# Kernel optimization log

Hardware: AMD Instinct MI355X
Metric: run time of the kernel (lower is better)

Reference implementation:

```python
import jax, jax.numpy as jnp
import numpy as np

BETA = 0.25
N_E = 8192
E_DIM = 256


def setup_inputs() -> dict:
    key = jax.random.key(0)
    k1, k2 = jax.random.split(key)
    z = jax.random.normal(k1, (16, E_DIM, 32, 32), dtype=jnp.float32)
    # matches torch init: uniform_(-1/n_e, 1/n_e)
    codebook = jax.random.uniform(k2, (N_E, E_DIM), dtype=jnp.float32,
                                  minval=-1.0 / N_E, maxval=1.0 / N_E)
    return {"z": z, "codebook": codebook}


def reference(z, codebook):
    B, C, H, W = z.shape  # C == e_dim
    zp = jnp.transpose(z, (0, 2, 3, 1))          # [B, H, W, C]
    zf = zp.reshape(-1, C)                       # [N, C], N = B*H*W
    # squared L2 distances: ||z||^2 + ||e||^2 - 2 z.e
    d = (jnp.sum(zf * zf, axis=1, keepdims=True)
         + jnp.sum(codebook * codebook, axis=1)
         - 2.0 * jnp.einsum('nc,kc->nk', zf, codebook))  # [N, n_e]
    min_encoding_indices = jnp.argmin(d, axis=1)         # [N]
    z_q = codebook[min_encoding_indices].reshape(zp.shape)  # [B, H, W, C]
    sg = jax.lax.stop_gradient
    loss = jnp.mean((sg(z_q) - zp) ** 2) + BETA * jnp.mean((z_q - sg(zp)) ** 2)
    # straight-through estimator
    z_q_st = zp + sg(z_q - zp)
    z_q_out = jnp.transpose(z_q_st, (0, 3, 1, 2))  # back to NCHW
    return z_q_out, loss, min_encoding_indices
```

## Files before the change

### kernel.cpp

```cpp
#include <hip/hip_runtime.h>

typedef short s8v __attribute__((ext_vector_type(8)));
typedef float f4v __attribute__((ext_vector_type(4)));
typedef float f4 __attribute__((ext_vector_type(4)));
typedef unsigned short u16v4 __attribute__((ext_vector_type(4)));

#define N_PIX 16384
#define NE    8192
#define EDIM  256
#define ZQ_ELEMS 4194304
#define MARGIN 4.5e-4f
#define NGRP 512

__device__ __forceinline__ float bf2f(unsigned short u) {
    union { unsigned int i; float f; } c; c.i = ((unsigned int)u) << 16; return c.f;
}
__device__ __forceinline__ unsigned short f2bf(float f) {
    unsigned int u = __float_as_uint(f);
    u = (u + 0x7fffu + ((u >> 16) & 1u)) >> 16;
    return (unsigned short)u;
}
__device__ __forceinline__ unsigned short f2bf_down(float f) {
    unsigned int u = __float_as_uint(f);
    unsigned short b = (unsigned short)(u >> 16);
    if ((u & 0xFFFFu) && (u >> 31)) b += 1;
    return b;
}

__device__ __forceinline__ float np_pw128sq(const float* a) {
    float r[8];
    #pragma unroll
    for (int j = 0; j < 8; ++j) r[j] = __fmul_rn(a[j], a[j]);
    for (int i = 8; i < 128; i += 8)
        #pragma unroll
        for (int j = 0; j < 8; ++j) r[j] = __fadd_rn(r[j], __fmul_rn(a[i + j], a[i + j]));
    return __fadd_rn(__fadd_rn(__fadd_rn(r[0], r[1]), __fadd_rn(r[2], r[3])),
                     __fadd_rn(__fadd_rn(r[4], r[5]), __fadd_rn(r[6], r[7])));
}


__global__ __launch_bounds__(256) void vq_prep(const float* __restrict__ cb,
                                               unsigned short* __restrict__ cb16,
                                               float* __restrict__ esum32) {
    int t = threadIdx.x;
    int base = blockIdx.x * 32;
    const float* src = cb + (size_t)base * EDIM;
    unsigned short* dst = cb16 + (size_t)base * EDIM;
    #pragma unroll
    for (int i = 0; i < 8; ++i) {
        int e0 = (i * 256 + t) * 4;
        f4 v = *(const f4*)(src + e0);
        u16v4 o;
        o.x = f2bf(v[0]); o.y = f2bf(v[1]); o.z = f2bf(v[2]); o.w = f2bf(v[3]);
        *(u16v4*)(dst + e0) = o;
    }
    if (t < 32) {
        const float* a = cb + (size_t)(base + t) * EDIM;
        esum32[base + t] = __fadd_rn(np_pw128sq(a), np_pw128sq(a + 128));
    }
}

__global__ __launch_bounds__(256) void vq_zprep(const float* __restrict__ z,
                                                unsigned short* __restrict__ z16) {
    __shared__ unsigned short zl[64 * 66];
    int t = threadIdx.x;
    int p0 = (blockIdx.x >> 2) * 64;
    int c0 = (blockIdx.x & 3) * 64;
    int b = p0 >> 10, hw0 = p0 & 1023;
    const float* src = z + (((size_t)b * 256 + c0) << 10) + hw0;
    #pragma unroll
    for (int i = 0; i < 16; ++i) {
        int idx = i * 256 + t;
        int ch = idx >> 6, px = idx & 63;
        zl[px * 66 + ch] = f2bf(src[((size_t)ch << 10) + px]);
    }
    __syncthreads();
    #pragma unroll
    for (int i = 0; i < 16; ++i) {
        int idx = i * 256 + t;
        int px = idx >> 6, ch = idx & 63;
        z16[((size_t)(p0 + px)) * 256 + c0 + ch] = zl[px * 66 + ch];
    }
}

__global__ __launch_bounds__(512, 2) void vq_phase1g(const unsigned short* __restrict__ cb16,
                                                     const unsigned short* __restrict__ z16,
                                                     unsigned short* __restrict__ gmin) {
    __shared__ unsigned short L[2][32768];
    const int t = threadIdx.x;
    const int wave = t >> 6, lane = t & 63;
    const int q = lane >> 4, r = lane & 15;
    const int wr = wave >> 2, wc = wave & 3;
    const int cm0 = ((int)blockIdx.x >> 3) * 256;
    const int pg  = (int)blockIdx.x & 7;

    const int pc0 = t, pc1 = t + 512;
    const int row0 = pc0 >> 2, row1 = pc1 >> 2;
    const int lc0 = (pc0 & 3) ^ ((row0 >> 1) & 3);
    const int lc1 = (pc1 & 3) ^ ((row1 >> 1) & 3);
    const int go0 = row0 * 256 + lc0 * 8;
    const int go1 = row1 * 256 + lc1 * 8;
    const int ld0 = pc0 * 8;
    const int ld1 = pc1 * 8;

    const unsigned short* gA = cb16 + (size_t)cm0 * 256;
    const unsigned short* gB0 = z16 + (size_t)pg * 2048 * 256;

    f4v acc[8][4];
    const f4v zz = {0.f, 0.f, 0.f, 0.f};
    #pragma unroll
    for (int mi = 0; mi < 8; ++mi)
        #pragma unroll
        for (int ni = 0; ni < 4; ++ni) acc[mi][ni] = zz;

    const int cxo = (q ^ ((r >> 1) & 3)) * 8;
    const int aro = (wr * 128 + r) * 32 + cxo;
    const int bro = 16384 + (wc * 64 + r) * 32 + cxo;

#define GLL(g, l) __builtin_amdgcn_global_load_lds( \
        (const __attribute__((address_space(1))) unsigned int*)(g), \
        (__attribute__((address_space(3))) unsigned int*)(l), 16, 0, 0)
#define STAGEKT(buf_, gk_, gBp_) do { \
        unsigned short* Lb = &L[(buf_)][0]; \
        GLL(gA + go0 + (gk_),            Lb + ld0); \
        GLL(gA + go1 + (gk_),            Lb + ld1); \
        GLL(gA + go0 + 32 + (gk_),       Lb + 8192 + ld0); \
        GLL(gA + go1 + 32 + (gk_),       Lb + 8192 + ld1); \
        GLL((gBp_) + go0 + (gk_),        Lb + 16384 + ld0); \
        GLL((gBp_) + go1 + (gk_),        Lb + 16384 + ld1); \
        GLL((gBp_) + go0 + 32 + (gk_),   Lb + 16384 + 8192 + ld0); \
        GLL((gBp_) + go1 + 32 + (gk_),   Lb + 16384 + 8192 + ld1); } while (0)
#define ARD(Lp, mi, ks) (*(const s8v*)&(Lp)[(ks) * 8192 + (mi) * 512 + aro])
#define BRD(Lp, ni, ks) (*(const s8v*)&(Lp)[(ks) * 8192 + (ni) * 512 + bro])
#define MFMA16(Aset, Bset, mo) do { \
        __builtin_amdgcn_s_setprio(1); \
        _Pragma("unroll") \
        for (int mi = 0; mi < 4; ++mi) \
            _Pragma("unroll") \
            for (int ni = 0; ni < 4; ++ni) \
                acc[(mo) + mi][ni] = __builtin_amdgcn_mfma_f32_16x16x32_bf16( \
                    Aset[mi], Bset[ni], acc[(mo) + mi][ni], 0, 0, 0); \
        __builtin_amdgcn_s_setprio(0); } while (0)

    STAGEKT(0, 0, gB0);
    asm volatile("s_waitcnt vmcnt(0)" ::: "memory");
    __builtin_amdgcn_s_barrier();
    s8v A0[4], A1[4], B0[4], B1[4];
    #pragma unroll
    for (int ni = 0; ni < 4; ++ni) B0[ni] = BRD(&L[0][0], ni, 0);
    #pragma unroll
    for (int mi = 0; mi < 4; ++mi) A0[mi] = ARD(&L[0][0], mi, 0);

    for (int it = 0; it < 32; ++it) {
        const int buf = it & 1;
        const unsigned short* Lb = &L[buf][0];
        const unsigned short* Ln = &L[buf ^ 1][0];
        const int nit = it + 1;
        const bool st = nit < 32;

        __builtin_amdgcn_s_barrier();
        if (st) STAGEKT(buf ^ 1, (nit & 3) * 64, gB0 + (size_t)(nit >> 2) * 65536);

        #pragma unroll
        for (int mi = 0; mi < 4; ++mi) A1[mi] = ARD(Lb, 4 + mi, 0);
        __builtin_amdgcn_sched_barrier(0);
        MFMA16(A0, B0, 0);

        #pragma unroll
        for (int mi = 0; mi < 4; ++mi) A0[mi] = ARD(Lb, mi, 1);
        #pragma unroll
        for (int ni = 0; ni < 4; ++ni) B1[ni] = BRD(Lb, ni, 1);
        __builtin_amdgcn_sched_barrier(0);
        MFMA16(A1, B0, 4);

        #pragma unroll
        for (int mi = 0; mi < 4; ++mi) A1[mi] = ARD(Lb, 4 + mi, 1);
        __builtin_amdgcn_sched_barrier(0);
        MFMA16(A0, B1, 0);

        if (st) {
            asm volatile("s_waitcnt vmcnt(0)" ::: "memory");
            __builtin_amdgcn_s_barrier();
            #pragma unroll
            for (int ni = 0; ni < 4; ++ni) B0[ni] = BRD(Ln, ni, 0);
            #pragma unroll
            for (int mi = 0; mi < 4; ++mi) A0[mi] = ARD(Ln, mi, 0);
        }
        __builtin_amdgcn_sched_barrier(0);
        MFMA16(A1, B1, 4);

        if ((it & 3) == 3) {
            const int pn0 = pg * 2048 + (it >> 2) * 256;
            #pragma unroll
            for (int mi = 0; mi < 8; ++mi) {
                int g = cm0 / 16 + wr * 8 + mi;
                #pragma unroll
                for (int ni = 0; ni < 4; ++ni) {
                    f4v a = acc[mi][ni];
                    float mx = fmaxf(fmaxf(a[0], a[1]), fmaxf(a[2], a[3]));
                    mx = fmaxf(mx, __shfl_xor(mx, 16));
                    mx = fmaxf(mx, __shfl_xor(mx, 32));
                    if (q == 0) {
                        int pxc = (pn0 + wc * 64 + ni * 16) >> 4;
                        gmin[(size_t)pxc * 8192 + g * 16 + r] = f2bf_down(-2.0f * mx);
                    }
                    acc[mi][ni] = zz;
                }
            }
        }
    }
#undef MFMA16
#undef BRD
#undef ARD
#undef STAGEKT
#undef GLL
}

__global__ __launch_bounds__(512, 2) void vq_phase1(const float* __restrict__ z,
                                                    const unsigned short* __restrict__ cb16,
                                                    unsigned short* __restrict__ gmin) {
    const int t = threadIdx.x;
    const int wave = t >> 6, lane = t & 63;
    const int col = lane & 15, q = lane >> 4;
    const int mb = (blockIdx.x >> 1) * 64;
    const int chalf = blockIdx.x & 1;

    s8v Z[4][8];
    #pragma unroll
    for (int pt = 0; pt < 4; ++pt) {
        int n = mb + pt * 16 + col;
        const float* zb = z + ((size_t)(n >> 10) << 18) + (size_t)(n & 1023);
        #pragma unroll
        for (int c0 = 0; c0 < 8; ++c0) {
            s8v a;
            #pragma unroll
            for (int j = 0; j < 8; ++j) {
                int c = c0 * 32 + q * 8 + j;
                a[j] = (short)f2bf(zb[(size_t)c << 10]);
            }
            Z[pt][c0] = a;
        }
    }

    const int kbase = chalf * 4096 + wave * 512;
    for (int it = 0; it < 16; ++it) {
        int n0 = kbase + it * 32;
        const unsigned short* bb = cb16 + (size_t)(n0 + col) * EDIM + q * 8;
        f4v zz = {0.f, 0.f, 0.f, 0.f};
        f4v acc[4][2];
        #pragma unroll
        for (int pt = 0; pt < 4; ++pt) { acc[pt][0] = zz; acc[pt][1] = zz; }
        #pragma unroll
        for (int c0 = 0; c0 < 8; ++c0) {
            s8v C0 = *(const s8v*)(bb + c0 * 32);
            s8v C1 = *(const s8v*)(bb + 16 * EDIM + c0 * 32);
            #pragma unroll
            for (int pt = 0; pt < 4; ++pt) {
                acc[pt][0] = __builtin_amdgcn_mfma_f32_16x16x32_bf16(C0, Z[pt][c0], acc[pt][0], 0, 0, 0);
                acc[pt][1] = __builtin_amdgcn_mfma_f32_16x16x32_bf16(C1, Z[pt][c0], acc[pt][1], 0, 0, 0);
            }
        }
        int gbase = chalf * 256 + wave * 32 + it * 2;
        #pragma unroll
        for (int pt = 0; pt < 4; ++pt) {
            #pragma unroll
            for (int s = 0; s < 2; ++s) {
                f4v a = acc[pt][s];
                float mx = fmaxf(fmaxf(a[0], a[1]), fmaxf(a[2], a[3]));
                mx = fmaxf(mx, __shfl_xor(mx, 16));
                mx = fmaxf(mx, __shfl_xor(mx, 32));
                if (q == 0)
                    gmin[(size_t)((mb >> 4) + pt) * 8192 + (gbase + s) * 16 + col] =
                        f2bf_down(-2.0f * mx);
            }
        }
    }
}

__global__ __launch_bounds__(256) void vq_phase2(const float* __restrict__ z,
                                                 const float* __restrict__ cb,
                                                 const float* __restrict__ esum32,
                                                 const unsigned short* __restrict__ gmin,
                                                 unsigned int* __restrict__ idxw) {
    __shared__ float zt[16 * 260];
    __shared__ unsigned short gm[NGRP * 17];
    __shared__ float zs[16];
    int t = threadIdx.x;
    int wave = t >> 6, lane = t & 63;
    int p0 = blockIdx.x * 16;
    int bb = p0 >> 10, inner = p0 & 1023;

    #pragma unroll
    for (int i = 0; i < 16; ++i) {
        int c = i * 16 + (t >> 4), p = t & 15;
        zt[p * 260 + c] = z[((size_t)(bb * 256 + c) << 10) + inner + p];
    }
    const unsigned short* gsrc = gmin + (size_t)blockIdx.x * 8192;
    #pragma unroll
    for (int j = 0; j < 4; ++j) {
        int li = (j * 256 + t) * 8;
        s8v v = *(const s8v*)(gsrc + li);
        int g = li >> 4, ph = li & 15;
        #pragma unroll
        for (int e = 0; e < 8; ++e) gm[g * 17 + ph + e] = (unsigned short)v[e];
    }
    __syncthreads();
    if (t < 16) {
        const float* a = zt + t * 260;
        zs[t] = __fadd_rn(np_pw128sq(a), np_pw128sq(a + 128));
    }
    __syncthreads();

    #pragma unroll
    for (int pp = 0; pp < 4; ++pp) {
        int p = wave * 4 + pp;
        float lmin = 3.0e38f;
        #pragma unroll
        for (int j = 0; j < 8; ++j) lmin = fminf(lmin, bf2f(gm[(lane * 8 + j) * 17 + p]));
        #pragma unroll
        for (int m = 1; m < 64; m <<= 1) lmin = fminf(lmin, __shfl_xor(lmin, m));
        float thr = lmin + MARGIN;
        float zsp = zs[p];

        float bd = 3.0e38f; int bk = 0x7FFFFFFF;
        for (int j = 0; j < 8; ++j) {
            unsigned long long mask = __ballot(bf2f(gm[(lane * 8 + j) * 17 + p]) <= thr);
            while (mask) {
                int lb = __builtin_ctzll(mask); mask &= mask - 1;
                int g = lb * 8 + j;
                int k = g * 16 + (lane >> 2);
                const f4* cr = (const f4*)(cb + (size_t)k * EDIM) + (lane & 3);
                const f4* zr = (const f4*)(zt + p * 260) + (lane & 3);
                double a0 = 0.0, a1 = 0.0, a2 = 0.0, a3 = 0.0;
                #pragma unroll
                for (int i = 0; i < 16; ++i) {
                    f4 x = zr[i * 4], y = cr[i * 4];
                    a0 = fma((double)x[0], (double)y[0], a0);
                    a1 = fma((double)x[1], (double)y[1], a1);
                    a2 = fma((double)x[2], (double)y[2], a2);
                    a3 = fma((double)x[3], (double)y[3], a3);
                }
                double s = (a0 + a1) + (a2 + a3);
                s += __shfl_xor(s, 1);
                s += __shfl_xor(s, 2);
                float E = (float)s;
                float d = __fsub_rn(__fadd_rn(zsp, esum32[k]), __fmul_rn(2.0f, E));
                if (d < bd || (d == bd && k < bk)) { bd = d; bk = k; }
            }
        }
        #pragma unroll
        for (int m = 1; m < 64; m <<= 1) {
            float od = __shfl_xor(bd, m); int ok = __shfl_xor(bk, m);
            if (od < bd || (od == bd && ok < bk)) { bd = od; bk = ok; }
        }
        if (lane == 0) idxw[p0 + p] = (unsigned int)bk;
    }
}

__global__ __launch_bounds__(256) void vq_emit(const float* __restrict__ cb,
                                               const float* __restrict__ z,
                                               const unsigned int* __restrict__ idxw,
                                               float* __restrict__ outf,
                                               float* __restrict__ lossw) {
    __shared__ float qrow[1024 * 17];
    __shared__ unsigned int lidx[1024];
    __shared__ float red[4];
    int t = threadIdx.x;
    int gtid = blockIdx.x * 256 + t;
    if (gtid < N_PIX) outf[ZQ_ELEMS + 1 + gtid] = (float)(idxw[gtid] & (NE - 1));

    int b = blockIdx.x >> 4;
    int c0 = (blockIdx.x & 15) * 16;

    #pragma unroll
    for (int j = 0; j < 4; ++j)
        lidx[j * 256 + t] = idxw[b * 1024 + j * 256 + t] & (NE - 1);
    __syncthreads();
    #pragma unroll
    for (int j = 0; j < 16; ++j) {
        int p = j * 64 + (t >> 2);
        f4 v = *(const f4*)(cb + (size_t)lidx[p] * EDIM + c0 + (t & 3) * 4);
        #pragma unroll
        for (int e = 0; e < 4; ++e) qrow[p * 17 + (t & 3) * 4 + e] = v[e];
    }
    __syncthreads();

    float acc = 0.f;
    size_t base = (size_t)blockIdx.x * 16384;
    for (int i = 0; i < 64; ++i) {
        size_t o = base + (size_t)i * 256 + t;
        int c = (int)((o >> 10) & 255);
        int p = (int)(o & 1023);
        float qv = qrow[p * 17 + (c - c0)];
        outf[o] = qv;
        float d = qv - z[o];
        acc = fmaf(d, d, acc);
    }
    #pragma unroll
    for (int off = 32; off > 0; off >>= 1) acc += __shfl_down(acc, off);
    if ((t & 63) == 0) red[t >> 6] = acc;
    __syncthreads();
    if (t == 0) atomicAdd(lossw, red[0] + red[1] + red[2] + red[3]);
}

__global__ void vq_finalize(const float* __restrict__ lossw, float* __restrict__ loss_out) {
    loss_out[0] = 1.25f * lossw[0] * (1.0f / 4194304.0f);
}

extern "C" void kernel_launch(void* const* d_in, const int* in_sizes, int n_in,
                              void* d_out, int out_size, void* d_ws, size_t ws_size,
                              hipStream_t stream) {
    const float* z  = (const float*)d_in[0];
    const float* cb = (const float*)d_in[1];
    float* outf = (float*)d_out;
    unsigned short* gmin = (unsigned short*)d_out;

    char* w = (char*)d_ws;
    unsigned short* cb16   = (unsigned short*)w;
    float*          esum32 = (float*)(w + 4194304);
    unsigned int*   idxw   = (unsigned int*)(w + 4227072);
    float*          lossw  = (float*)(w + 4292608);
    unsigned short* z16    = (unsigned short*)(w + 4292864);

    if (ws_size < 4292612) return;
    const bool big_ws = (ws_size >= 12681472);

    hipMemsetAsync(lossw, 0, sizeof(float), stream);
    vq_prep    <<<NE / 32, 256, 0, stream>>>(cb, cb16, esum32);
    if (big_ws) {
        vq_zprep  <<<(N_PIX / 64) * (EDIM / 64), 256, 0, stream>>>(z, z16);
        vq_phase1g<<<(NE / 256) * (N_PIX / 2048), 512, 0, stream>>>(cb16, z16, gmin);
    } else {
        vq_phase1 <<<(N_PIX / 64) * 2, 512, 0, stream>>>(z, cb16, gmin);
    }
    vq_phase2  <<<N_PIX / 16, 256, 0, stream>>>(z, cb, esum32, gmin, idxw);
    vq_emit    <<<256, 256, 0, stream>>>(cb, z, idxw, outf, lossw);
    vq_finalize<<<1, 1, 0, stream>>>(lossw, outf + ZQ_ELEMS);
}
```

Measured before the change: 263.8 us.

## Merge prep kernels, move loss into phase2, vectorize emit writes, drop finalize

Combines the codebook and z bf16 prep kernels into one launch and vectorizes the z transpose loads and stores. The loss sum moves into phase2, which already holds z in shared memory and knows the chosen index, and is accumulated with a double atomic. This lets emit skip re-reading z and write its output as contiguous float4. The separate finalize kernel is dropped because emit now writes the loss. The cost is one extra codebook row read per pixel in phase2 and more atomics.

```diff
diff --git a/kernel.cpp b/kernel.cpp
--- a/kernel.cpp
+++ b/kernel.cpp
@@ -39,47 +39,55 @@
 }
 
 
-__global__ __launch_bounds__(256) void vq_prep(const float* __restrict__ cb,
-                                               unsigned short* __restrict__ cb16,
-                                               float* __restrict__ esum32) {
-    int t = threadIdx.x;
-    int base = blockIdx.x * 32;
-    const float* src = cb + (size_t)base * EDIM;
-    unsigned short* dst = cb16 + (size_t)base * EDIM;
-    #pragma unroll
-    for (int i = 0; i < 8; ++i) {
-        int e0 = (i * 256 + t) * 4;
-        f4 v = *(const f4*)(src + e0);
-        u16v4 o;
-        o.x = f2bf(v[0]); o.y = f2bf(v[1]); o.z = f2bf(v[2]); o.w = f2bf(v[3]);
-        *(u16v4*)(dst + e0) = o;
-    }
-    if (t < 32) {
-        const float* a = cb + (size_t)(base + t) * EDIM;
-        esum32[base + t] = __fadd_rn(np_pw128sq(a), np_pw128sq(a + 128));
-    }
-}
-
-__global__ __launch_bounds__(256) void vq_zprep(const float* __restrict__ z,
-                                                unsigned short* __restrict__ z16) {
+__global__ __launch_bounds__(256) void vq_pre(const float* __restrict__ z,
+                                              const float* __restrict__ cb,
+                                              unsigned short* __restrict__ z16,
+                                              unsigned short* __restrict__ cb16,
+                                              float* __restrict__ esum32,
+                                              int do_z) {
     __shared__ unsigned short zl[64 * 66];
     int t = threadIdx.x;
-    int p0 = (blockIdx.x >> 2) * 64;
-    int c0 = (blockIdx.x & 3) * 64;
-    int b = p0 >> 10, hw0 = p0 & 1023;
-    const float* src = z + (((size_t)b * 256 + c0) << 10) + hw0;
-    #pragma unroll
-    for (int i = 0; i < 16; ++i) {
-        int idx = i * 256 + t;
-        int ch = idx >> 6, px = idx & 63;
-        zl[px * 66 + ch] = f2bf(src[((size_t)ch << 10) + px]);
-    }
-    __syncthreads();
-    #pragma unroll
-    for (int i = 0; i < 16; ++i) {
-        int idx = i * 256 + t;
-        int px = idx >> 6, ch = idx & 63;
-        z16[((size_t)(p0 + px)) * 256 + c0 + ch] = zl[px * 66 + ch];
+    int bx = blockIdx.x;
+    if (bx < 1024) {
+        if (!do_z) return;
+        int p0 = (bx >> 2) * 64;
+        int c0 = (bx & 3) * 64;
+        int b = p0 >> 10, hw0 = p0 & 1023;
+        const float* src = z + (((size_t)b * 256 + c0) << 10) + hw0;
+        #pragma unroll
+        for (int i = 0; i < 4; ++i) {
+            int idx = i * 256 + t;
+            int ch = idx >> 4, pq = idx & 15;
+            f4 v = *(const f4*)(src + ((size_t)ch << 10) + pq * 4);
+            #pragma unroll
+            for (int e = 0; e < 4; ++e) zl[(pq * 4 + e) * 66 + ch] = f2bf(v[e]);
+        }
+        __syncthreads();
+        #pragma unroll
+        for (int i = 0; i < 2; ++i) {
+            int idx = i * 256 + t;
+            int px = idx >> 3, cc = idx & 7;
+            s8v o;
+            #pragma unroll
+            for (int e = 0; e < 8; ++e) o[e] = (short)zl[px * 66 + cc * 8 + e];
+            *(s8v*)&z16[((size_t)(p0 + px)) * 256 + c0 + cc * 8] = o;
+        }
+    } else {
+        int base = (bx - 1024) * 32;
+        const float* src = cb + (size_t)base * EDIM;
+        unsigned short* dst = cb16 + (size_t)base * EDIM;
+        #pragma unroll
+        for (int i = 0; i < 8; ++i) {
+            int e0 = (i * 256 + t) * 4;
+            f4 v = *(const f4*)(src + e0);
+            u16v4 o;
+            o.x = f2bf(v[0]); o.y = f2bf(v[1]); o.z = f2bf(v[2]); o.w = f2bf(v[3]);
+            *(u16v4*)(dst + e0) = o;
+        }
+        if (t < 32) {
+            const float* a = cb + (size_t)(base + t) * EDIM;
+            esum32[base + t] = __fadd_rn(np_pw128sq(a), np_pw128sq(a + 128));
+        }
     }
 }
 
@@ -281,7 +289,8 @@
                                                  const float* __restrict__ cb,
                                                  const float* __restrict__ esum32,
                                                  const unsigned short* __restrict__ gmin,
-                                                 unsigned int* __restrict__ idxw) {
+                                                 unsigned int* __restrict__ idxw,
+                                                 double* __restrict__ lossd) {
     __shared__ float zt[16 * 260];
     __shared__ unsigned short gm[NGRP * 17];
     __shared__ float zs[16];
@@ -311,6 +320,7 @@
     }
     __syncthreads();
 
+    float wls = 0.f;
     #pragma unroll
     for (int pp = 0; pp < 4; ++pp) {
         int p = wave * 4 + pp;
@@ -354,20 +364,30 @@
             if (od < bd || (od == bd && ok < bk)) { bd = od; bk = ok; }
         }
         if (lane == 0) idxw[p0 + p] = (unsigned int)bk;
-    }
+
+        f4 cv = *(const f4*)(cb + (size_t)bk * EDIM + lane * 4);
+        f4 zv = *(const f4*)(zt + p * 260 + lane * 4);
+        float s0 = 0.f;
+        #pragma unroll
+        for (int e = 0; e < 4; ++e) { float dx = cv[e] - zv[e]; s0 = fmaf(dx, dx, s0); }
+        #pragma unroll
+        for (int m = 1; m < 64; m <<= 1) s0 += __shfl_xor(s0, m);
+        wls += s0;
+    }
+    if (lane == 0) atomicAdd(lossd, (double)wls);
 }
 
 __global__ __launch_bounds__(256) void vq_emit(const float* __restrict__ cb,
-                                               const float* __restrict__ z,
                                                const unsigned int* __restrict__ idxw,
-                                               float* __restrict__ outf,
-                                               float* __restrict__ lossw) {
+                                               const double* __restrict__ lossd,
+                                               float* __restrict__ outf) {
     __shared__ float qrow[1024 * 17];
     __shared__ unsigned int lidx[1024];
-    __shared__ float red[4];
     int t = threadIdx.x;
     int gtid = blockIdx.x * 256 + t;
     if (gtid < N_PIX) outf[ZQ_ELEMS + 1 + gtid] = (float)(idxw[gtid] & (NE - 1));
+    if (blockIdx.x == 0 && t == 0)
+        outf[ZQ_ELEMS] = 1.25f * (float)(lossd[0] * (1.0 / 4194304.0));
 
     int b = blockIdx.x >> 4;
     int c0 = (blockIdx.x & 15) * 16;
@@ -385,26 +405,14 @@
     }
     __syncthreads();
 
-    float acc = 0.f;
     size_t base = (size_t)blockIdx.x * 16384;
-    for (int i = 0; i < 64; ++i) {
-        size_t o = base + (size_t)i * 256 + t;
-        int c = (int)((o >> 10) & 255);
-        int p = (int)(o & 1023);
-        float qv = qrow[p * 17 + (c - c0)];
-        outf[o] = qv;
-        float d = qv - z[o];
-        acc = fmaf(d, d, acc);
-    }
-    #pragma unroll
-    for (int off = 32; off > 0; off >>= 1) acc += __shfl_down(acc, off);
-    if ((t & 63) == 0) red[t >> 6] = acc;
-    __syncthreads();
-    if (t == 0) atomicAdd(lossw, red[0] + red[1] + red[2] + red[3]);
-}
-
-__global__ void vq_finalize(const float* __restrict__ lossw, float* __restrict__ loss_out) {
-    loss_out[0] = 1.25f * lossw[0] * (1.0f / 4194304.0f);
+    #pragma unroll
+    for (int i = 0; i < 16; ++i) {
+        f4 v;
+        #pragma unroll
+        for (int e = 0; e < 4; ++e) v[e] = qrow[(t * 4 + e) * 17 + i];
+        *(f4*)&outf[base + (size_t)i * 1024 + t * 4] = v;
+    }
 }
 
 extern "C" void kernel_launch(void* const* d_in, const int* in_sizes, int n_in,
@@ -419,21 +427,19 @@
     unsigned short* cb16   = (unsigned short*)w;
     float*          esum32 = (float*)(w + 4194304);
     unsigned int*   idxw   = (unsigned int*)(w + 4227072);
-    float*          lossw  = (float*)(w + 4292608);
+    double*         lossd  = (double*)(w + 4292608);
     unsigned short* z16    = (unsigned short*)(w + 4292864);
 
-    if (ws_size < 4292612) return;
+    if (ws_size < 4292616) return;
     const bool big_ws = (ws_size >= 12681472);
 
-    hipMemsetAsync(lossw, 0, sizeof(float), stream);
-    vq_prep    <<<NE / 32, 256, 0, stream>>>(cb, cb16, esum32);
+    hipMemsetAsync(lossd, 0, sizeof(double), stream);
+    vq_pre<<<1280, 256, 0, stream>>>(z, cb, z16, cb16, esum32, big_ws ? 1 : 0);
     if (big_ws) {
-        vq_zprep  <<<(N_PIX / 64) * (EDIM / 64), 256, 0, stream>>>(z, z16);
         vq_phase1g<<<(NE / 256) * (N_PIX / 2048), 512, 0, stream>>>(cb16, z16, gmin);
     } else {
         vq_phase1 <<<(N_PIX / 64) * 2, 512, 0, stream>>>(z, cb16, gmin);
     }
-    vq_phase2  <<<N_PIX / 16, 256, 0, stream>>>(z, cb, esum32, gmin, idxw);
-    vq_emit    <<<256, 256, 0, stream>>>(cb, z, idxw, outf, lossw);
-    vq_finalize<<<1, 1, 0, stream>>>(lossw, outf + ZQ_ELEMS);
-}
+    vq_phase2  <<<N_PIX / 16, 256, 0, stream>>>(z, cb, esum32, gmin, idxw, lossd);
+    vq_emit    <<<256, 256, 0, stream>>>(cb, idxw, lossd, outf);
+}
```

Measured after the change: 322.5 us. 22.3% more time.

## Merge codebook and z prep kernels, vectorize loads, widen phase2 blocks

Applied to the files above, without the earlier changes.

Merges the codebook bf16 conversion and the z transpose/convert into one launch, using a block-index split, so one kernel launch goes away. The z transpose now uses float4 global loads and 16-byte stores. vq_phase2 goes from 256 to 512 threads per block, so each wave handles 2 pixels instead of 4, and its z tile load is vectorized. The risks are more LDS bank conflicts from the strided shared-memory writes and changed occupancy in phase2.

```diff
diff --git a/kernel.cpp b/kernel.cpp
--- a/kernel.cpp
+++ b/kernel.cpp
@@ -39,47 +39,55 @@
 }
 
 
-__global__ __launch_bounds__(256) void vq_prep(const float* __restrict__ cb,
-                                               unsigned short* __restrict__ cb16,
-                                               float* __restrict__ esum32) {
-    int t = threadIdx.x;
-    int base = blockIdx.x * 32;
-    const float* src = cb + (size_t)base * EDIM;
-    unsigned short* dst = cb16 + (size_t)base * EDIM;
-    #pragma unroll
-    for (int i = 0; i < 8; ++i) {
-        int e0 = (i * 256 + t) * 4;
-        f4 v = *(const f4*)(src + e0);
-        u16v4 o;
-        o.x = f2bf(v[0]); o.y = f2bf(v[1]); o.z = f2bf(v[2]); o.w = f2bf(v[3]);
-        *(u16v4*)(dst + e0) = o;
-    }
-    if (t < 32) {
-        const float* a = cb + (size_t)(base + t) * EDIM;
-        esum32[base + t] = __fadd_rn(np_pw128sq(a), np_pw128sq(a + 128));
-    }
-}
-
-__global__ __launch_bounds__(256) void vq_zprep(const float* __restrict__ z,
-                                                unsigned short* __restrict__ z16) {
+__global__ __launch_bounds__(256) void vq_pre(const float* __restrict__ z,
+                                              const float* __restrict__ cb,
+                                              unsigned short* __restrict__ z16,
+                                              unsigned short* __restrict__ cb16,
+                                              float* __restrict__ esum32,
+                                              int do_z) {
     __shared__ unsigned short zl[64 * 66];
     int t = threadIdx.x;
-    int p0 = (blockIdx.x >> 2) * 64;
-    int c0 = (blockIdx.x & 3) * 64;
-    int b = p0 >> 10, hw0 = p0 & 1023;
-    const float* src = z + (((size_t)b * 256 + c0) << 10) + hw0;
-    #pragma unroll
-    for (int i = 0; i < 16; ++i) {
-        int idx = i * 256 + t;
-        int ch = idx >> 6, px = idx & 63;
-        zl[px * 66 + ch] = f2bf(src[((size_t)ch << 10) + px]);
-    }
-    __syncthreads();
-    #pragma unroll
-    for (int i = 0; i < 16; ++i) {
-        int idx = i * 256 + t;
-        int px = idx >> 6, ch = idx & 63;
-        z16[((size_t)(p0 + px)) * 256 + c0 + ch] = zl[px * 66 + ch];
+    int bx = blockIdx.x;
+    if (bx < 1024) {
+        if (!do_z) return;
+        int p0 = (bx >> 2) * 64;
+        int c0 = (bx & 3) * 64;
+        int b = p0 >> 10, hw0 = p0 & 1023;
+        const float* src = z + (((size_t)b * 256 + c0) << 10) + hw0;
+        #pragma unroll
+        for (int i = 0; i < 4; ++i) {
+            int idx = i * 256 + t;
+            int ch = idx >> 4, pq = idx & 15;
+            f4 v = *(const f4*)(src + ((size_t)ch << 10) + pq * 4);
+            #pragma unroll
+            for (int e = 0; e < 4; ++e) zl[(pq * 4 + e) * 66 + ch] = f2bf(v[e]);
+        }
+        __syncthreads();
+        #pragma unroll
+        for (int i = 0; i < 2; ++i) {
+            int idx = i * 256 + t;
+            int px = idx >> 3, cc = idx & 7;
+            s8v o;
+            #pragma unroll
+            for (int e = 0; e < 8; ++e) o[e] = (short)zl[px * 66 + cc * 8 + e];
+            *(s8v*)&z16[((size_t)(p0 + px)) * 256 + c0 + cc * 8] = o;
+        }
+    } else {
+        int base = (bx - 1024) * 32;
+        const float* src = cb + (size_t)base * EDIM;
+        unsigned short* dst = cb16 + (size_t)base * EDIM;
+        #pragma unroll
+        for (int i = 0; i < 8; ++i) {
+            int e0 = (i * 256 + t) * 4;
+            f4 v = *(const f4*)(src + e0);
+            u16v4 o;
+            o.x = f2bf(v[0]); o.y = f2bf(v[1]); o.z = f2bf(v[2]); o.w = f2bf(v[3]);
+            *(u16v4*)(dst + e0) = o;
+        }
+        if (t < 32) {
+            const float* a = cb + (size_t)(base + t) * EDIM;
+            esum32[base + t] = __fadd_rn(np_pw128sq(a), np_pw128sq(a + 128));
+        }
     }
 }
 
@@ -277,11 +285,11 @@
     }
 }
 
-__global__ __launch_bounds__(256) void vq_phase2(const float* __restrict__ z,
-                                                 const float* __restrict__ cb,
-                                                 const float* __restrict__ esum32,
-                                                 const unsigned short* __restrict__ gmin,
-                                                 unsigned int* __restrict__ idxw) {
+__global__ __launch_bounds__(512, 2) void vq_phase2(const float* __restrict__ z,
+                                                    const float* __restrict__ cb,
+                                                    const float* __restrict__ esum32,
+                                                    const unsigned short* __restrict__ gmin,
+                                                    unsigned int* __restrict__ idxw) {
     __shared__ float zt[16 * 260];
     __shared__ unsigned short gm[NGRP * 17];
     __shared__ float zs[16];
@@ -290,17 +298,21 @@
     int p0 = blockIdx.x * 16;
     int bb = p0 >> 10, inner = p0 & 1023;
 
-    #pragma unroll
-    for (int i = 0; i < 16; ++i) {
-        int c = i * 16 + (t >> 4), p = t & 15;
-        zt[p * 260 + c] = z[((size_t)(bb * 256 + c) << 10) + inner + p];
+    const float* zb = z + (((size_t)bb * 256) << 10) + inner;
+    #pragma unroll
+    for (int i = 0; i < 2; ++i) {
+        int job = i * 512 + t;
+        int c = job >> 2, q4 = job & 3;
+        f4 v = *(const f4*)(zb + ((size_t)c << 10) + q4 * 4);
+        #pragma unroll
+        for (int e = 0; e < 4; ++e) zt[(q4 * 4 + e) * 260 + c] = v[e];
     }
     const unsigned short* gsrc = gmin + (size_t)blockIdx.x * 8192;
     #pragma unroll
-    for (int j = 0; j < 4; ++j) {
-        int li = (j * 256 + t) * 8;
-        s8v v = *(const s8v*)(gsrc + li);
-        int g = li >> 4, ph = li & 15;
+    for (int i = 0; i < 2; ++i) {
+        int li8 = (i * 512 + t) * 8;
+        s8v v = *(const s8v*)(gsrc + li8);
+        int g = li8 >> 4, ph = li8 & 15;
         #pragma unroll
         for (int e = 0; e < 8; ++e) gm[g * 17 + ph + e] = (unsigned short)v[e];
     }
@@ -312,8 +324,8 @@
     __syncthreads();
 
     #pragma unroll
-    for (int pp = 0; pp < 4; ++pp) {
-        int p = wave * 4 + pp;
+    for (int pp = 0; pp < 2; ++pp) {
+        int p = wave * 2 + pp;
         float lmin = 3.0e38f;
         #pragma unroll
         for (int j = 0; j < 8; ++j) lmin = fminf(lmin, bf2f(gm[(lane * 8 + j) * 17 + p]));
@@ -422,18 +434,17 @@
     float*          lossw  = (float*)(w + 4292608);
     unsigned short* z16    = (unsigned short*)(w + 4292864);
 
-    if (ws_size < 4292612) return;
+    if (ws_size < 4292864) return;
     const bool big_ws = (ws_size >= 12681472);
 
     hipMemsetAsync(lossw, 0, sizeof(float), stream);
-    vq_prep    <<<NE / 32, 256, 0, stream>>>(cb, cb16, esum32);
+    vq_pre<<<1280, 256, 0, stream>>>(z, cb, z16, cb16, esum32, big_ws ? 1 : 0);
     if (big_ws) {
-        vq_zprep  <<<(N_PIX / 64) * (EDIM / 64), 256, 0, stream>>>(z, z16);
         vq_phase1g<<<(NE / 256) * (N_PIX / 2048), 512, 0, stream>>>(cb16, z16, gmin);
     } else {
         vq_phase1 <<<(N_PIX / 64) * 2, 512, 0, stream>>>(z, cb16, gmin);
     }
-    vq_phase2  <<<N_PIX / 16, 256, 0, stream>>>(z, cb, esum32, gmin, idxw);
+    vq_phase2  <<<N_PIX / 16, 512, 0, stream>>>(z, cb, esum32, gmin, idxw);
     vq_emit    <<<256, 256, 0, stream>>>(cb, z, idxw, outf, lossw);
     vq_finalize<<<1, 1, 0, stream>>>(lossw, outf + ZQ_ELEMS);
 }
```

Result: slower. 317.7 us (+20.4%).
